# Optimization experiments

Hardware: AMD Instinct MI355X
Metric: run time of the kernel (lower is better)

## Reference

```python
import jax, jax.numpy as jnp
import numpy as np

B, H, S, D = 4, 16, 2048, 64

def setup_inputs() -> dict:
    key = jax.random.key(0)
    kq, kk, kv = jax.random.split(key, 3)
    Q = jax.random.normal(kq, (B, H, S, D), dtype=jnp.float32)
    K = jax.random.normal(kk, (B, H, S, D), dtype=jnp.float32)
    V = jax.random.normal(kv, (B, H, S, D), dtype=jnp.float32)
    return {"Q": Q, "K": K, "V": V}

def reference(Q, K, V):
    # Faithful to the source: NO 1/sqrt(d) scaling.
    # scores: [B, H, S, S]
    scores = jnp.einsum("bhqd,bhkd->bhqk", Q, K)
    probs = jax.nn.softmax(scores, axis=-1)
    # output: [B, H, S, D]
    return jnp.einsum("bhqk,bhkd->bhqd", probs, V)
```

## Files before the change

kernel.cpp:

```cpp
#include <hip/hip_runtime.h>
#include <hip/hip_bf16.h>
#include <math.h>

typedef _Float16 f16x8 __attribute__((ext_vector_type(8)));
typedef _Float16 f16x4 __attribute__((ext_vector_type(4)));
typedef __fp16   hf4  __attribute__((ext_vector_type(4)));
typedef float    f32x4 __attribute__((ext_vector_type(4)));
typedef __bf16   bf16x8 __attribute__((ext_vector_type(8)));
typedef __bf16   bf16x4 __attribute__((ext_vector_type(4)));

#define MFMA32_F16(a,b,c)  __builtin_amdgcn_mfma_f32_16x16x32_f16((a),(b),(c),0,0,0)
#define MFMA_BF16(a,b,c)   __builtin_amdgcn_mfma_f32_16x16x32_bf16((a),(b),(c),0,0,0)

constexpr int S_LEN = 2048;
constexpr int DH    = 64;
constexpr int KBLK  = 64;
constexpr int NSTEP = S_LEN / KBLK;
constexpr float LOG2E = 1.44269504088896340736f;
constexpr size_t TILE_BYTES = 16384;
constexpr size_t WS_NEED = 64ull * NSTEP * TILE_BYTES;

__device__ __forceinline__ void gload16(const void* g, void* l) {
    __builtin_amdgcn_global_load_lds(
        (const __attribute__((address_space(1))) void*)g,
        (__attribute__((address_space(3))) void*)l, 16, 0, 0);
}

__device__ __forceinline__ float exp2_fast(float x) {
    float r;
    asm("v_exp_f32 %0, %1" : "=v"(r) : "v"(x));
    return r;
}

__device__ __forceinline__ float redmax_lg(float x) {
    x = fmaxf(x, __shfl_xor(x, 16));
    x = fmaxf(x, __shfl_xor(x, 32));
    return x;
}

__device__ __forceinline__ f16x4 as_f16x4(hf4 h) {
    f16x4 f;
    __builtin_memcpy(&f, &h, 8);
    return f;
}

__global__ __launch_bounds__(256)
void prep_kernel(const float* __restrict__ Kg, const float* __restrict__ Vg,
                 unsigned char* __restrict__ ws)
{
    __shared__ _Float16 sT[64 * 70];

    const int blk = blockIdx.x;
    const int tid = threadIdx.x;
    const float* Kt = Kg + (size_t)blk * KBLK * DH;
    const float* Vt = Vg + (size_t)blk * KBLK * DH;
    char* wK = (char*)(ws + (size_t)blk * TILE_BYTES);
    char* wV = wK + 8192;

    #pragma unroll
    for (int c = 0; c < 2; ++c) {
        const int eid = tid + c * 256;
        const int row = eid >> 3;
        const int d0  = (eid & 7) * 8;
        f32x4 a = *(const f32x4*)(Kt + row * DH + d0);
        f32x4 b = *(const f32x4*)(Kt + row * DH + d0 + 4);
        f16x8 h;
        #pragma unroll
        for (int j = 0; j < 4; ++j) { h[j] = (_Float16)a[j]; h[4 + j] = (_Float16)b[j]; }
        const int koff = (row * 128 + d0 * 2) ^ ((row & 7) << 4);
        *(f16x8*)(wK + koff) = h;
        f32x4 va = *(const f32x4*)(Vt + row * DH + d0);
        f32x4 vb = *(const f32x4*)(Vt + row * DH + d0 + 4);
        #pragma unroll
        for (int j = 0; j < 4; ++j) {
            sT[row * 70 + d0 + j]     = (_Float16)va[j];
            sT[row * 70 + d0 + 4 + j] = (_Float16)vb[j];
        }
    }
    __syncthreads();
    #pragma unroll
    for (int c = 0; c < 2; ++c) {
        const int id  = tid + c * 256;
        const int p   = id >> 8;
        const int lgc = (id >> 6) & 3;
        const int d   = id & 63;
        const int kv0 = p * 32 + lgc * 4;
        f16x8 h;
        #pragma unroll
        for (int j = 0; j < 4; ++j) {
            h[j]     = sT[(kv0 + j) * 70 + d];
            h[4 + j] = sT[(kv0 + 16 + j) * 70 + d];
        }
        *(f16x8*)(wV + (p * 4 + lgc) * 1024 + d * 16) = h;
    }
}

__global__ __launch_bounds__(256, 4)
void attn_main(const float* __restrict__ Qg0, const unsigned char* __restrict__ ws,
               float* __restrict__ Og0)
{
    __shared__ __align__(16) _Float16 sK[2][KBLK * DH];
    __shared__ __align__(16) _Float16 sV[2][KBLK * DH];

    const int tid  = threadIdx.x;
    const int lane = tid & 63;
    const int w    = tid >> 6;
    const int lg   = lane >> 4;
    const int li   = lane & 15;
    const int X    = (li & 7) << 4;

    const int n   = blockIdx.x;
    const int xcd = n & 7;
    const int m_  = n >> 3;
    const int bh  = xcd * 8 + (m_ >> 4);
    const int qp  = m_ & 15;

    const float* Qg = Qg0 + (size_t)bh * S_LEN * DH;
    float*       Og = Og0 + (size_t)bh * S_LEN * DH;
    const unsigned char* wsb = ws + (size_t)bh * NSTEP * TILE_BYTES;

    f16x8 qA[2], qB[2];
    {
        const int qrowA = qp * 128 + w * 16 + li;
        const float* pa = Qg + (size_t)qrowA * DH;
        const float* pb = pa + 64 * DH;
        #pragma unroll
        for (int f = 0; f < 2; ++f) {
            f32x4 a0 = *(const f32x4*)(pa + f * 32 + lg * 8);
            f32x4 a1 = *(const f32x4*)(pa + f * 32 + lg * 8 + 4);
            f32x4 b0 = *(const f32x4*)(pb + f * 32 + lg * 8);
            f32x4 b1 = *(const f32x4*)(pb + f * 32 + lg * 8 + 4);
            #pragma unroll
            for (int j = 0; j < 4; ++j) {
                qA[f][j]     = (_Float16)(a0[j] * LOG2E);
                qA[f][4 + j] = (_Float16)(a1[j] * LOG2E);
                qB[f][j]     = (_Float16)(b0[j] * LOG2E);
                qB[f][4 + j] = (_Float16)(b1[j] * LOG2E);
            }
        }
    }

    f16x8 ones;
    #pragma unroll
    for (int j = 0; j < 8; ++j) ones[j] = (_Float16)1.0f;

    f32x4 accoA[4], accoB[4];
    #pragma unroll
    for (int t = 0; t < 4; ++t) {
        accoA[t] = f32x4{0.f, 0.f, 0.f, 0.f};
        accoB[t] = f32x4{0.f, 0.f, 0.f, 0.f};
    }
    float mA = 0.f, mB = 0.f;
    f32x4 laccA = {0.f, 0.f, 0.f, 0.f};
    f32x4 laccB = {0.f, 0.f, 0.f, 0.f};

    auto stage = [&](int buf, int t) {
        const unsigned char* src = wsb + (size_t)t * TILE_BYTES;
        char* lk = (char*)&sK[buf][0] + w * 2048;
        char* lv = (char*)&sV[buf][0] + w * 2048;
        const unsigned char* gk = src + w * 2048 + lane * 16;
        const unsigned char* gv = src + 8192 + w * 2048 + lane * 16;
        gload16(gk,        lk);
        gload16(gk + 1024, lk + 1024);
        gload16(gv,        lv);
        gload16(gv + 1024, lv + 1024);
    };

    stage(0, 0);
    __syncthreads();
    int buf = 0;

    for (int t = 0; t < NSTEP; ++t) {
        if (t + 1 < NSTEP) stage(buf ^ 1, t + 1);

        const char* kb = (const char*)&sK[buf][0];
        const char* vb = (const char*)&sV[buf][0];

        f32x4 sA[4], sB[4];
        const f32x4 cA = {-mA, -mA, -mA, -mA};
        const f32x4 cB = {-mB, -mB, -mB, -mB};
        __builtin_amdgcn_s_setprio(1);
        #pragma unroll
        for (int t4 = 0; t4 < 4; ++t4) {
            const char* kr = kb + t4 * 2048 + li * 128;
            f16x8 kf0 = *(const f16x8*)(kr + ((0 * 64 + lg * 16) ^ X));
            f16x8 kf1 = *(const f16x8*)(kr + ((1 * 64 + lg * 16) ^ X));
            f32x4 a = MFMA32_F16(kf0, qA[0], cA);
            a       = MFMA32_F16(kf1, qA[1], a);
            f32x4 b = MFMA32_F16(kf0, qB[0], cB);
            b       = MFMA32_F16(kf1, qB[1], b);
            sA[t4] = a;
            sB[t4] = b;
        }
        __builtin_amdgcn_s_setprio(0);

        float mlA = fmaxf(fmaxf(fmaxf(sA[0][0], sA[0][1]), sA[0][2]),
                          fmaxf(fmaxf(sA[0][3], sA[1][0]), sA[1][1]));
        mlA = fmaxf(mlA, fmaxf(fmaxf(sA[1][2], sA[1][3]), sA[2][0]));
        mlA = fmaxf(mlA, fmaxf(fmaxf(sA[2][1], sA[2][2]), sA[2][3]));
        mlA = fmaxf(mlA, fmaxf(fmaxf(sA[3][0], sA[3][1]), fmaxf(sA[3][2], sA[3][3])));
        float mlB = fmaxf(fmaxf(fmaxf(sB[0][0], sB[0][1]), sB[0][2]),
                          fmaxf(fmaxf(sB[0][3], sB[1][0]), sB[1][1]));
        mlB = fmaxf(mlB, fmaxf(fmaxf(sB[1][2], sB[1][3]), sB[2][0]));
        mlB = fmaxf(mlB, fmaxf(fmaxf(sB[2][1], sB[2][2]), sB[2][3]));
        mlB = fmaxf(mlB, fmaxf(fmaxf(sB[3][0], sB[3][1]), fmaxf(sB[3][2], sB[3][3])));

        if (__any(mlA > 8.f)) {
            const float rowmax = redmax_lg(mlA);
            const float delta  = fmaxf(rowmax, 0.f);
            const float sc     = exp2_fast(-delta);
            mA += delta;  laccA *= sc;
            #pragma unroll
            for (int t4 = 0; t4 < 4; ++t4) { accoA[t4] *= sc; sA[t4] -= delta; }
        }
        if (__any(mlB > 8.f)) {
            const float rowmax = redmax_lg(mlB);
            const float delta  = fmaxf(rowmax, 0.f);
            const float sc     = exp2_fast(-delta);
            mB += delta;  laccB *= sc;
            #pragma unroll
            for (int t4 = 0; t4 < 4; ++t4) { accoB[t4] *= sc; sB[t4] -= delta; }
        }

        f16x4 pA[4], pB[4];
        #pragma unroll
        for (int t4 = 0; t4 < 4; ++t4) {
            float a0 = exp2_fast(sA[t4][0]);
            float a1 = exp2_fast(sA[t4][1]);
            float a2 = exp2_fast(sA[t4][2]);
            float a3 = exp2_fast(sA[t4][3]);
            pA[t4] = as_f16x4(__builtin_shufflevector(
                __builtin_amdgcn_cvt_pkrtz(a0, a1),
                __builtin_amdgcn_cvt_pkrtz(a2, a3), 0, 1, 2, 3));
            float b0 = exp2_fast(sB[t4][0]);
            float b1 = exp2_fast(sB[t4][1]);
            float b2 = exp2_fast(sB[t4][2]);
            float b3 = exp2_fast(sB[t4][3]);
            pB[t4] = as_f16x4(__builtin_shufflevector(
                __builtin_amdgcn_cvt_pkrtz(b0, b1),
                __builtin_amdgcn_cvt_pkrtz(b2, b3), 0, 1, 2, 3));
        }

        f16x8 pfA0 = __builtin_shufflevector(pA[0], pA[1], 0, 1, 2, 3, 4, 5, 6, 7);
        f16x8 pfA1 = __builtin_shufflevector(pA[2], pA[3], 0, 1, 2, 3, 4, 5, 6, 7);
        f16x8 pfB0 = __builtin_shufflevector(pB[0], pB[1], 0, 1, 2, 3, 4, 5, 6, 7);
        f16x8 pfB1 = __builtin_shufflevector(pB[2], pB[3], 0, 1, 2, 3, 4, 5, 6, 7);

        __builtin_amdgcn_s_setprio(1);
        laccA = MFMA32_F16(ones, pfA0, laccA);
        laccB = MFMA32_F16(ones, pfB0, laccB);
        #pragma unroll
        for (int t4v = 0; t4v < 4; ++t4v) {
            f16x8 vv0 = *(const f16x8*)(vb + lg * 1024 + t4v * 256 + li * 16);
            accoA[t4v] = MFMA32_F16(vv0, pfA0, accoA[t4v]);
            accoB[t4v] = MFMA32_F16(vv0, pfB0, accoB[t4v]);
            f16x8 vv1 = *(const f16x8*)(vb + 4096 + lg * 1024 + t4v * 256 + li * 16);
            accoA[t4v] = MFMA32_F16(vv1, pfA1, accoA[t4v]);
            accoB[t4v] = MFMA32_F16(vv1, pfB1, accoB[t4v]);
        }
        laccA = MFMA32_F16(ones, pfA1, laccA);
        laccB = MFMA32_F16(ones, pfB1, laccB);
        __builtin_amdgcn_s_setprio(0);

        __syncthreads();
        buf ^= 1;
    }

    {
        const int qrowA = qp * 128 + w * 16 + li;
        const float ia = 1.f / laccA[0];
        const float ib = 1.f / laccB[0];
        float* oa = Og + (size_t)qrowA * DH;
        float* ob = oa + 64 * DH;
        #pragma unroll
        for (int t4 = 0; t4 < 4; ++t4) {
            f32x4 o1, o2;
            #pragma unroll
            for (int r = 0; r < 4; ++r) { o1[r] = accoA[t4][r] * ia; o2[r] = accoB[t4][r] * ib; }
            *(f32x4*)(oa + t4 * 16 + lg * 4) = o1;
            *(f32x4*)(ob + t4 * 16 + lg * 4) = o2;
        }
    }
}

__global__ __launch_bounds__(256)
void attn_fwd_kernel(const float* __restrict__ Qg0,
                     const float* __restrict__ Kg0,
                     const float* __restrict__ Vg0,
                     float* __restrict__ Og0)
{
    constexpr int VT_P = 72;
    constexpr int P_PB = 72;
    __shared__ __align__(16) __bf16 sKh[KBLK * DH];
    __shared__ __align__(16) __bf16 sKl[KBLK * DH];
    __shared__ __align__(16) __bf16 sVt[DH * VT_P];
    __shared__ __align__(16) __bf16 sP[4][16 * P_PB];

    const int tid  = threadIdx.x;
    const int lane = tid & 63;
    const int w    = tid >> 6;
    const int lg   = lane >> 4;
    const int li   = lane & 15;

    const int n   = blockIdx.x;
    const int xcd = n & 7;
    const int m   = n >> 3;
    const int bh  = xcd * 8 + (m >> 5);
    const int qt  = m & 31;

    const float* Qg = Qg0 + (size_t)bh * S_LEN * DH;
    const float* Kg = Kg0 + (size_t)bh * S_LEN * DH;
    const float* Vg = Vg0 + (size_t)bh * S_LEN * DH;
    float*       Og = Og0 + (size_t)bh * S_LEN * DH;

    bf16x8 qh[2], ql[2];
    {
        const int qrow = qt * 64 + w * 16 + li;
        const float* qp = Qg + (size_t)qrow * DH;
        #pragma unroll
        for (int f = 0; f < 2; ++f) {
            const int dbase = f * 32 + lg * 8;
            #pragma unroll
            for (int j = 0; j < 8; ++j) {
                float q = qp[dbase + j];
                __bf16 h = (__bf16)q;
                qh[f][j] = h;
                ql[f][j] = (__bf16)(q - (float)h);
            }
        }
    }

    f32x4 acco[4];
    #pragma unroll
    for (int t = 0; t < 4; ++t) acco[t] = f32x4{0.f, 0.f, 0.f, 0.f};
    float mval[4], lval[4];
    #pragma unroll
    for (int r = 0; r < 4; ++r) { mval[r] = -INFINITY; lval[r] = 0.f; }

    for (int step = 0; step < NSTEP; ++step) {
        __syncthreads();
        {
            const int kv0 = step * KBLK;
            #pragma unroll
            for (int i = 0; i < 4; ++i) {
                const int f4 = tid + i * 256;
                const int kv = f4 >> 4;
                const int d4 = (f4 & 15) << 2;
                f32x4 kvec = *(const f32x4*)(Kg + (size_t)(kv0 + kv) * DH + d4);
                bf16x4 h, l;
                #pragma unroll
                for (int j = 0; j < 4; ++j) {
                    __bf16 hh = (__bf16)kvec[j];
                    h[j] = hh;
                    l[j] = (__bf16)(kvec[j] - (float)hh);
                }
                const int idx = (kv * DH + d4) ^ ((kv & 7) << 3);
                *(bf16x4*)&sKh[idx] = h;
                *(bf16x4*)&sKl[idx] = l;
                f32x4 vvec = *(const f32x4*)(Vg + (size_t)(kv0 + kv) * DH + d4);
                #pragma unroll
                for (int j = 0; j < 4; ++j)
                    sVt[(d4 + j) * VT_P + kv] = (__bf16)vvec[j];
            }
        }
        __syncthreads();

        f32x4 accs[4];
        #pragma unroll
        for (int t4 = 0; t4 < 4; ++t4) {
            f32x4 acc = f32x4{0.f, 0.f, 0.f, 0.f};
            const int row = t4 * 16 + li;
            #pragma unroll
            for (int f = 0; f < 2; ++f) {
                const int idx = (row * DH + f * 32 + lg * 8) ^ ((row & 7) << 3);
                bf16x8 kh = *(const bf16x8*)&sKh[idx];
                bf16x8 kl = *(const bf16x8*)&sKl[idx];
                acc = MFMA_BF16(qh[f], kh, acc);
                acc = MFMA_BF16(qh[f], kl, acc);
                acc = MFMA_BF16(ql[f], kh, acc);
            }
            accs[t4] = acc;
        }

        #pragma unroll
        for (int r = 0; r < 4; ++r) {
            float mx = fmaxf(fmaxf(accs[0][r], accs[1][r]), fmaxf(accs[2][r], accs[3][r]));
            #pragma unroll
            for (int msk = 1; msk <= 8; msk <<= 1)
                mx = fmaxf(mx, __shfl_xor(mx, msk));
            const float newm  = fmaxf(mval[r], mx);
            const float scale = __expf(mval[r] - newm);
            mval[r] = newm;
            lval[r] *= scale;
            #pragma unroll
            for (int t4 = 0; t4 < 4; ++t4) acco[t4][r] *= scale;
            float s = 0.f;
            #pragma unroll
            for (int t4 = 0; t4 < 4; ++t4) {
                float p = __expf(accs[t4][r] - newm);
                accs[t4][r] = p;
                s += p;
            }
            #pragma unroll
            for (int msk = 1; msk <= 8; msk <<= 1)
                s += __shfl_xor(s, msk);
            lval[r] += s;
        }

        #pragma unroll
        for (int r = 0; r < 4; ++r) {
            const int rr = lg * 4 + r;
            #pragma unroll
            for (int t4 = 0; t4 < 4; ++t4)
                sP[w][rr * P_PB + t4 * 16 + li] = (__bf16)accs[t4][r];
        }

        bf16x8 pa[2];
        #pragma unroll
        for (int f = 0; f < 2; ++f)
            pa[f] = *(const bf16x8*)&sP[w][li * P_PB + f * 32 + lg * 8];
        #pragma unroll
        for (int t4 = 0; t4 < 4; ++t4) {
            #pragma unroll
            for (int f = 0; f < 2; ++f) {
                bf16x8 vb = *(const bf16x8*)&sVt[(t4 * 16 + li) * VT_P + f * 32 + lg * 8];
                acco[t4] = MFMA_BF16(pa[f], vb, acco[t4]);
            }
        }
    }

    {
        const int qrow0 = qt * 64 + w * 16;
        #pragma unroll
        for (int r = 0; r < 4; ++r) {
            const int rr = lg * 4 + r;
            const float inv = 1.f / lval[r];
            #pragma unroll
            for (int t4 = 0; t4 < 4; ++t4)
                Og[(size_t)(qrow0 + rr) * DH + t4 * 16 + li] = acco[t4][r] * inv;
        }
    }
}

extern "C" void kernel_launch(void* const* d_in, const int* in_sizes, int n_in,
                              void* d_out, int out_size, void* d_ws, size_t ws_size,
                              hipStream_t stream) {
    const float* Q = (const float*)d_in[0];
    const float* K = (const float*)d_in[1];
    const float* V = (const float*)d_in[2];
    float* O = (float*)d_out;
    if (ws_size >= WS_NEED) {
        prep_kernel<<<dim3(2048), dim3(256), 0, stream>>>(K, V, (unsigned char*)d_ws);
        attn_main<<<dim3(1024), dim3(256), 0, stream>>>(Q, (const unsigned char*)d_ws, O);
    } else {
        attn_fwd_kernel<<<dim3(2048), dim3(256), 0, stream>>>(Q, K, V, O);
    }
}
```

Measured before the change: 100.7 us.

## Split KV sequence across two blocks per query tile with merge kernel

Adds a split-KV (flash-decoding style) path: each query tile is processed by two blocks, each covering half of the key/value steps, writing unnormalized partial outputs plus max and sum to workspace. A new merge kernel rescales and combines the two partials into the final output. This doubles the grid from 1024 to 2048 blocks to improve CU occupancy and load balance, at the cost of extra global writes and reads of partial outputs and a third kernel launch. The path only runs when the workspace is large enough.

```diff
diff --git a/kernel.cpp b/kernel.cpp
--- a/kernel.cpp
+++ b/kernel.cpp
@@ -16,9 +16,15 @@
 constexpr int DH    = 64;
 constexpr int KBLK  = 64;
 constexpr int NSTEP = S_LEN / KBLK;
+constexpr int ROWS  = 64 * S_LEN;
 constexpr float LOG2E = 1.44269504088896340736f;
 constexpr size_t TILE_BYTES = 16384;
-constexpr size_t WS_NEED = 64ull * NSTEP * TILE_BYTES;
+constexpr size_t WS_MID = 64ull * NSTEP * TILE_BYTES;
+constexpr size_t OP_OFF  = WS_MID;
+constexpr size_t OP_SIZE = 2ull * ROWS * DH * 4;
+constexpr size_t ML_OFF  = OP_OFF + OP_SIZE;
+constexpr size_t ML_SIZE = 2ull * ROWS * 8;
+constexpr size_t WS_SPLIT = ML_OFF + ML_SIZE;
 
 __device__ __forceinline__ void gload16(const void* g, void* l) {
     __builtin_amdgcn_global_load_lds(
@@ -95,9 +101,10 @@
     }
 }
 
+template <int SPLIT>
 __global__ __launch_bounds__(256, 4)
-void attn_main(const float* __restrict__ Qg0, const unsigned char* __restrict__ ws,
-               float* __restrict__ Og0)
+void attn_body(const float* __restrict__ Qg0, const unsigned char* __restrict__ ws,
+               float* __restrict__ Og0, float* __restrict__ Op, float2* __restrict__ mlG)
 {
     __shared__ __align__(16) _Float16 sK[2][KBLK * DH];
     __shared__ __align__(16) _Float16 sV[2][KBLK * DH];
@@ -112,12 +119,20 @@
     const int n   = blockIdx.x;
     const int xcd = n & 7;
     const int m_  = n >> 3;
-    const int bh  = xcd * 8 + (m_ >> 4);
-    const int qp  = m_ & 15;
+    int bh, qp, half;
+    if (SPLIT) {
+        bh   = xcd * 8 + (m_ >> 5);
+        qp   = (m_ & 31) >> 1;
+        half = m_ & 1;
+    } else {
+        bh   = xcd * 8 + (m_ >> 4);
+        qp   = m_ & 15;
+        half = 0;
+    }
+    const int nstep = SPLIT ? (NSTEP / 2) : NSTEP;
 
     const float* Qg = Qg0 + (size_t)bh * S_LEN * DH;
-    float*       Og = Og0 + (size_t)bh * S_LEN * DH;
-    const unsigned char* wsb = ws + (size_t)bh * NSTEP * TILE_BYTES;
+    const unsigned char* wsb = ws + ((size_t)bh * NSTEP + (size_t)half * (NSTEP / 2)) * TILE_BYTES;
 
     f16x8 qA[2], qB[2];
     {
@@ -170,8 +185,8 @@
     __syncthreads();
     int buf = 0;
 
-    for (int t = 0; t < NSTEP; ++t) {
-        if (t + 1 < NSTEP) stage(buf ^ 1, t + 1);
+    for (int t = 0; t < nstep; ++t) {
+        if (t + 1 < nstep) stage(buf ^ 1, t + 1);
 
         const char* kb = (const char*)&sK[buf][0];
         const char* vb = (const char*)&sV[buf][0];
@@ -266,7 +281,22 @@
         buf ^= 1;
     }
 
-    {
+    if (SPLIT) {
+        const int rowA = bh * S_LEN + qp * 128 + w * 16 + li;
+        const int rowB = rowA + 64;
+        float* oa = Op + (size_t)half * ROWS * DH + (size_t)rowA * DH;
+        float* ob = oa + 64 * DH;
+        #pragma unroll
+        for (int t4 = 0; t4 < 4; ++t4) {
+            *(f32x4*)(oa + t4 * 16 + lg * 4) = accoA[t4];
+            *(f32x4*)(ob + t4 * 16 + lg * 4) = accoB[t4];
+        }
+        if (lg == 0) {
+            mlG[(size_t)half * ROWS + rowA] = float2{mA, laccA[0]};
+            mlG[(size_t)half * ROWS + rowB] = float2{mB, laccB[0]};
+        }
+    } else {
+        float* Og = Og0 + (size_t)bh * S_LEN * DH;
         const int qrowA = qp * 128 + w * 16 + li;
         const float ia = 1.f / laccA[0];
         const float ib = 1.f / laccB[0];
@@ -280,6 +310,35 @@
             *(f32x4*)(oa + t4 * 16 + lg * 4) = o1;
             *(f32x4*)(ob + t4 * 16 + lg * 4) = o2;
         }
+    }
+}
+
+__global__ __launch_bounds__(256)
+void merge_kernel(const float* __restrict__ Op, const float2* __restrict__ mlG,
+                  float* __restrict__ Og)
+{
+    const int tid = threadIdx.x;
+    const int row = blockIdx.x * 64 + (tid >> 2);
+    const int seg = (tid & 3) * 16;
+    const float2 p0 = mlG[row];
+    const float2 p1 = mlG[ROWS + row];
+    const float mm  = fmaxf(p0.x, p1.x);
+    float sc0 = exp2_fast(p0.x - mm);
+    float sc1 = exp2_fast(p1.x - mm);
+    const float inv = 1.f / (sc0 * p0.y + sc1 * p1.y);
+    sc0 *= inv;
+    sc1 *= inv;
+    const float* a = Op + (size_t)row * DH + seg;
+    const float* b = a + (size_t)ROWS * DH;
+    float* o = Og + (size_t)row * DH + seg;
+    #pragma unroll
+    for (int i = 0; i < 4; ++i) {
+        f32x4 x = *(const f32x4*)(a + i * 4);
+        f32x4 y = *(const f32x4*)(b + i * 4);
+        f32x4 r;
+        #pragma unroll
+        for (int j = 0; j < 4; ++j) r[j] = x[j] * sc0 + y[j] * sc1;
+        *(f32x4*)(o + i * 4) = r;
     }
 }
 
@@ -449,9 +508,16 @@
     const float* K = (const float*)d_in[1];
     const float* V = (const float*)d_in[2];
     float* O = (float*)d_out;
-    if (ws_size >= WS_NEED) {
+    if (ws_size >= WS_SPLIT) {
+        unsigned char* ws = (unsigned char*)d_ws;
+        float*  Op = (float*)(ws + OP_OFF);
+        float2* ml = (float2*)(ws + ML_OFF);
+        prep_kernel<<<dim3(2048), dim3(256), 0, stream>>>(K, V, ws);
+        attn_body<1><<<dim3(2048), dim3(256), 0, stream>>>(Q, ws, nullptr, Op, ml);
+        merge_kernel<<<dim3(2048), dim3(256), 0, stream>>>(Op, ml, O);
+    } else if (ws_size >= WS_MID) {
         prep_kernel<<<dim3(2048), dim3(256), 0, stream>>>(K, V, (unsigned char*)d_ws);
-        attn_main<<<dim3(1024), dim3(256), 0, stream>>>(Q, (const unsigned char*)d_ws, O);
+        attn_body<0><<<dim3(1024), dim3(256), 0, stream>>>(Q, (const unsigned char*)d_ws, O, nullptr, nullptr);
     } else {
         attn_fwd_kernel<<<dim3(2048), dim3(256), 0, stream>>>(Q, K, V, O);
     }
```

After: 122.3 us. 21.5% more time.

## Triple-buffer K/V tiles with prefetch distance two and partial vmcnt waits

Applied to the files above, without the earlier changes.

Moves from double to triple buffering of the K/V LDS tiles, issuing the async global-to-LDS loads two steps ahead. The end-of-iteration full sync becomes a partial s_waitcnt vmcnt(4) plus barrier, so the loads for the next-next tile stay in flight while the next tile is consumed. This is meant to hide more global-load latency behind the MFMA work. In exchange LDS use rises from 32KB to 48KB per block and launch bounds drop to 3 blocks per CU, which lowers occupancy.

```diff
diff --git a/kernel.cpp b/kernel.cpp
--- a/kernel.cpp
+++ b/kernel.cpp
@@ -95,12 +95,12 @@
     }
 }
 
-__global__ __launch_bounds__(256, 4)
+__global__ __launch_bounds__(256, 3)
 void attn_main(const float* __restrict__ Qg0, const unsigned char* __restrict__ ws,
                float* __restrict__ Og0)
 {
-    __shared__ __align__(16) _Float16 sK[2][KBLK * DH];
-    __shared__ __align__(16) _Float16 sV[2][KBLK * DH];
+    __shared__ __align__(16) _Float16 sK[3][KBLK * DH];
+    __shared__ __align__(16) _Float16 sV[3][KBLK * DH];
 
     const int tid  = threadIdx.x;
     const int lane = tid & 63;
@@ -154,10 +154,10 @@
     f32x4 laccA = {0.f, 0.f, 0.f, 0.f};
     f32x4 laccB = {0.f, 0.f, 0.f, 0.f};
 
-    auto stage = [&](int buf, int t) {
+    auto stage = [&](char* lkb, char* lvb, int t) {
         const unsigned char* src = wsb + (size_t)t * TILE_BYTES;
-        char* lk = (char*)&sK[buf][0] + w * 2048;
-        char* lv = (char*)&sV[buf][0] + w * 2048;
+        char* lk = lkb + w * 2048;
+        char* lv = lvb + w * 2048;
         const unsigned char* gk = src + w * 2048 + lane * 16;
         const unsigned char* gv = src + 8192 + w * 2048 + lane * 16;
         gload16(gk,        lk);
@@ -166,15 +166,21 @@
         gload16(gv + 1024, lv + 1024);
     };
 
-    stage(0, 0);
-    __syncthreads();
-    int buf = 0;
+    char* krp = (char*)&sK[0][0]; char* vrp = (char*)&sV[0][0];
+    char* knp = (char*)&sK[1][0]; char* vnp = (char*)&sV[1][0];
+    char* kwp = (char*)&sK[2][0]; char* vwp = (char*)&sV[2][0];
+
+    stage(krp, vrp, 0);
+    stage(knp, vnp, 1);
+    asm volatile("s_waitcnt vmcnt(4)" ::: "memory");
+    __builtin_amdgcn_s_barrier();
+    __builtin_amdgcn_sched_barrier(0);
 
     for (int t = 0; t < NSTEP; ++t) {
-        if (t + 1 < NSTEP) stage(buf ^ 1, t + 1);
-
-        const char* kb = (const char*)&sK[buf][0];
-        const char* vb = (const char*)&sV[buf][0];
+        if (t + 2 < NSTEP) stage(kwp, vwp, t + 2);
+
+        const char* kb = krp;
+        const char* vb = vrp;
 
         f32x4 sA[4], sB[4];
         const f32x4 cA = {-mA, -mA, -mA, -mA};
@@ -262,8 +268,16 @@
         laccB = MFMA32_F16(ones, pfB1, laccB);
         __builtin_amdgcn_s_setprio(0);
 
-        __syncthreads();
-        buf ^= 1;
+        if (t + 2 < NSTEP) {
+            asm volatile("s_waitcnt vmcnt(4)" ::: "memory");
+        } else {
+            asm volatile("s_waitcnt vmcnt(0)" ::: "memory");
+        }
+        __builtin_amdgcn_s_barrier();
+        __builtin_amdgcn_sched_barrier(0);
+
+        char* tk = krp; krp = knp; knp = kwp; kwp = tk;
+        char* tv = vrp; vrp = vnp; vnp = vwp; vwp = tv;
     }
 
     {
```

Result: slower. 105.4 us (+4.7%).
